# Kernel tuning notes

Measured on AMD Instinct MI355X. Metric: run time of the kernel, lower is better.

## Reference

```python
import jax, jax.numpy as jnp
import numpy as np

N = 4096      # num nodes/docs (<= max_compare=5000, so no random subsampling)
IN = 768      # input feature dim
OUT = 512     # projector output dim
TEM = 0.5     # temperature
BN_EPS = 1e-5
NORM_EPS = 1e-12


def setup_inputs() -> dict:
    key = jax.random.key(0)
    ks = jax.random.split(key, 5)
    doc0 = jax.random.normal(ks[0], (N, IN), dtype=jnp.float32)
    doc1 = jax.random.normal(ks[1], (N, IN), dtype=jnp.float32)
    doc2 = jax.random.normal(ks[2], (N, IN), dtype=jnp.float32)
    # 6 freshly-initialized projectors (one per view per pair, as in the torch forward)
    W1s = jax.random.normal(ks[3], (6, IN, OUT), dtype=jnp.float32) * 0.05
    b1s = jnp.zeros((6, OUT), dtype=jnp.float32)
    gammas = jnp.ones((6, OUT), dtype=jnp.float32)
    betas = jnp.zeros((6, OUT), dtype=jnp.float32)
    W2s = jax.random.normal(ks[4], (6, OUT, OUT), dtype=jnp.float32) * 0.05
    b2s = jnp.zeros((6, OUT), dtype=jnp.float32)
    return {"doc0": doc0, "doc1": doc1, "doc2": doc2,
            "W1s": W1s, "b1s": b1s, "gammas": gammas, "betas": betas,
            "W2s": W2s, "b2s": b2s}


def _projector(x, W1, b1, g, b, W2, b2):
    # Linear -> BatchNorm1d (training-mode batch stats) -> ReLU -> Linear
    h = x @ W1 + b1
    mu = h.mean(axis=0)
    var = h.var(axis=0)  # biased, matching torch BN normalization
    h = (h - mu) * jax.lax.rsqrt(var + BN_EPS) * g + b
    h = jax.nn.relu(h)
    return h @ W2 + b2


def _l2norm(x):
    n = jnp.sqrt(jnp.sum(x * x, axis=1, keepdims=True))
    return x / jnp.maximum(n, NORM_EPS)


def _pair_loss(a, b):
    # a, b: [N, OUT], already L2-normalized.
    # Full-matrix form of the chunked batch_loss (mathematically identical).
    refl = jnp.exp((a @ a.T) / TEM)      # [N, N]
    between = jnp.exp((a @ b.T) / TEM)   # [N, N]
    pos = jnp.diagonal(between)
    denom = refl.sum(axis=1) + between.sum(axis=1) - jnp.diagonal(refl)
    return -jnp.log(pos / denom)


def reference(doc0, doc1, doc2, W1s, b1s, gammas, betas, W2s, b2s):
    docs = [doc0, doc1, doc2]
    pairs = [(0, 1), (0, 2), (1, 2)]
    total = jnp.float32(0.0)
    k = 0
    for (i, j) in pairs:
        o1 = _l2norm(_projector(docs[i], W1s[k], b1s[k], gammas[k], betas[k], W2s[k], b2s[k]))
        k += 1
        o2 = _l2norm(_projector(docs[j], W1s[k], b1s[k], gammas[k], betas[k], W2s[k], b2s[k]))
        k += 1
        l = 0.5 * (_pair_loss(o1, o2) + _pair_loss(o2, o1))
        total = total + l.mean()
    return total / 3.0
```

## Files before the change

### kernel.cpp

```cpp
#include <hip/hip_runtime.h>
#include <hip/hip_bf16.h>
#include <hip/hip_fp8.h>

#define N_ROWS 4096
#define IN_DIM 768
#define OUT_DIM 512


using bf16x8 = __attribute__((ext_vector_type(8))) short;
using f32x4  = __attribute__((ext_vector_type(4))) float;
using i64    = long;
using i64x2  = __attribute__((ext_vector_type(2))) long;

__device__ __constant__ int c_docmap[6] = {0, 1, 0, 2, 1, 2};

__device__ inline unsigned short f2bf(float f) {
    __hip_bfloat16 h = __float2bfloat16(f);
    return reinterpret_cast<unsigned short&>(h);
}
__device__ inline float bf2f(unsigned short u) {
    return __uint_as_float((unsigned int)u << 16);
}
__device__ inline unsigned char f2fp8(float f) {
    __hip_fp8_e4m3 t(f);
    return t.__x;
}
__device__ inline uint4 pack8bf(const float* v) {
    uint4 o;
    unsigned short* p = (unsigned short*)&o;
#pragma unroll
    for (int j = 0; j < 8; ++j) p[j] = f2bf(v[j]);
    return o;
}

__global__ __launch_bounds__(256) void prep(
    const float* __restrict__ d0, const float* __restrict__ d1,
    const float* __restrict__ d2, const float* __restrict__ W1s,
    const float* __restrict__ W2s, unsigned short* __restrict__ Xb,
    unsigned short* __restrict__ W1t, unsigned short* __restrict__ W2t,
    char* __restrict__ zbase) {
    int wunit = blockIdx.x * 4 + (threadIdx.x >> 6);
    int lane = threadIdx.x & 63;
    int lane15 = lane & 15, quad = lane >> 4;
    if (wunit < 18432) {
        int d = wunit / 6144, u = wunit % 6144;
        int gt = u / 24, kf = u % 24;
        const float* src = (d == 0) ? d0 : ((d == 1) ? d1 : d2);
        const float* s = src + (size_t)(gt * 16 + lane15) * IN_DIM + kf * 32 + quad * 8;
        float4 a = *(const float4*)s, b = *(const float4*)(s + 4);
        float v[8] = {a.x, a.y, a.z, a.w, b.x, b.y, b.z, b.w};
        *(uint4*)(Xb + (size_t)d * N_ROWS * IN_DIM + (size_t)u * 512 + lane * 8) = pack8bf(v);
    } else if (wunit < 23040) {
        int v0 = wunit - 18432;
        int z = v0 / 768, u = v0 % 768;
        int gt = u / 24, kf = u % 24;
        int n = gt * 16 + lane15;
        int k0 = kf * 32 + quad * 8;
        const float* W = W1s + (size_t)z * IN_DIM * OUT_DIM;
        float v[8];
#pragma unroll
        for (int j = 0; j < 8; ++j) v[j] = W[(size_t)(k0 + j) * OUT_DIM + n];
        *(uint4*)(W1t + (size_t)z * OUT_DIM * IN_DIM + (size_t)u * 512 + lane * 8) = pack8bf(v);
    } else if (wunit < 26112) {
        int v0 = wunit - 23040;
        int z = v0 / 512, u = v0 % 512;
        int gt = u / 16, kf = u % 16;
        int n = gt * 16 + lane15;
        int k0 = kf * 32 + quad * 8;
        const float* W = W2s + (size_t)z * OUT_DIM * OUT_DIM;
        float v[8];
#pragma unroll
        for (int j = 0; j < 8; ++j) v[j] = W[(size_t)(k0 + j) * OUT_DIM + n];
        *(uint4*)(W2t + (size_t)z * OUT_DIM * OUT_DIM + (size_t)u * 512 + lane * 8) = pack8bf(v);
    } else {
        size_t b = (size_t)(wunit - 26112) * 1024 + (size_t)lane * 16;
        if (b < (size_t)(24576 + 98304))
            *(float4*)(zbase + b) = (float4){0.f, 0.f, 0.f, 0.f};
    }
}

__global__ __launch_bounds__(256) void gemm1_bn(
    const unsigned short* __restrict__ Xb, const unsigned short* __restrict__ W1t,
    const float* __restrict__ biasAll, unsigned short* __restrict__ H,
    float* __restrict__ stats) {
    const int NKF = IN_DIM / 32;
    int px = blockIdx.x;
    int logical = (px & 7) * 96 + (px >> 3);
    int T = logical >> 1, sub = logical & 1;
    int z = T >> 6, rem = T & 63;
    int m0 = (rem >> 2) * 256, n0 = (rem & 3) * 128;
    const unsigned short* A = Xb + (size_t)c_docmap[z] * N_ROWS * IN_DIM;
    const unsigned short* B = W1t + (size_t)z * OUT_DIM * IN_DIM;
    const float* bz = biasAll + (size_t)z * OUT_DIM;
    unsigned short* C = H + (size_t)z * N_ROWS * OUT_DIM;

    int tid = threadIdx.x;
    int wave = (tid >> 6) + sub * 4, lane = tid & 63;
    int lane15 = lane & 15, quad = lane >> 4;
    int wrow = (wave >> 1) * 64, wcol = (wave & 1) * 64;

    const unsigned short* Ca = A + (size_t)((m0 + wrow) >> 4) * NKF * 512 + (size_t)lane * 8;
    const unsigned short* Cb = B + (size_t)((n0 + wcol) >> 4) * NKF * 512 + (size_t)lane * 8;

    f32x4 acc[4][4];
#pragma unroll
    for (int mt = 0; mt < 4; ++mt)
#pragma unroll
        for (int nt = 0; nt < 4; ++nt)
            acc[mt][nt] = (f32x4){0.f, 0.f, 0.f, 0.f};

    bf16x8 aC[4], bC[4], aN[4], bN[4];
#pragma unroll
    for (int t = 0; t < 4; ++t) {
        aC[t] = *(const bf16x8*)(Ca + (size_t)t * NKF * 512);
        bC[t] = *(const bf16x8*)(Cb + (size_t)t * NKF * 512);
    }
#pragma unroll
    for (int kf = 0; kf < NKF; ++kf) {
        if (kf < NKF - 1) {
#pragma unroll
            for (int t = 0; t < 4; ++t) {
                aN[t] = *(const bf16x8*)(Ca + (size_t)t * NKF * 512 + (kf + 1) * 512);
                bN[t] = *(const bf16x8*)(Cb + (size_t)t * NKF * 512 + (kf + 1) * 512);
            }
        }
        __builtin_amdgcn_s_setprio(1);
#pragma unroll
        for (int mt = 0; mt < 4; ++mt)
#pragma unroll
            for (int nt = 0; nt < 4; ++nt)
                acc[mt][nt] = __builtin_amdgcn_mfma_f32_16x16x32_bf16(aC[mt], bC[nt], acc[mt][nt], 0, 0, 0);
        __builtin_amdgcn_s_setprio(0);
#pragma unroll
        for (int t = 0; t < 4; ++t) { aC[t] = aN[t]; bC[t] = bN[t]; }
    }

    float s1[4] = {0.f, 0.f, 0.f, 0.f}, s2[4] = {0.f, 0.f, 0.f, 0.f};
#pragma unroll
    for (int nt = 0; nt < 4; ++nt) {
        int col = n0 + wcol + nt * 16 + lane15;
        float bv = bz[col];
#pragma unroll
        for (int mt = 0; mt < 4; ++mt)
#pragma unroll
            for (int r = 0; r < 4; ++r) {
                int row = m0 + wrow + mt * 16 + quad * 4 + r;
                float v = acc[mt][nt][r] + bv;
                C[(size_t)row * OUT_DIM + col] = f2bf(v);
                s1[nt] += v; s2[nt] += v * v;
            }
    }
#pragma unroll
    for (int nt = 0; nt < 4; ++nt) {
        float a = s1[nt], b = s2[nt];
        a += __shfl_xor(a, 16); a += __shfl_xor(a, 32);
        b += __shfl_xor(b, 16); b += __shfl_xor(b, 32);
        if (quad == 0) {
            int col = n0 + wcol + nt * 16 + lane15;
            atomicAdd(&stats[((size_t)z * OUT_DIM + col) * 2 + 0], a);
            atomicAdd(&stats[((size_t)z * OUT_DIM + col) * 2 + 1], b);
        }
    }
}

__global__ __launch_bounds__(256) void bn_apply(
    const unsigned short* __restrict__ H, unsigned short* __restrict__ Hb,
    const float* __restrict__ stats, const float* __restrict__ gammas,
    const float* __restrict__ betas) {
    int wunit = blockIdx.x * 4 + (threadIdx.x >> 6);
    if (wunit >= 24576) return;
    int lane = threadIdx.x & 63;
    int lane15 = lane & 15, quad = lane >> 4;
    int z = wunit / 4096, u = wunit % 4096;
    int gt = u / 16, kf = u % 16;
    int row = gt * 16 + lane15;
    int k = kf * 32 + quad * 8;
    uint4 hu = *(const uint4*)(H + ((size_t)z * N_ROWS + row) * OUT_DIM + k);
    unsigned int w[4] = {hu.x, hu.y, hu.z, hu.w};
    float v[8];
#pragma unroll
    for (int j = 0; j < 8; ++j) {
        unsigned short us = (j & 1) ? (unsigned short)(w[j >> 1] >> 16)
                                    : (unsigned short)(w[j >> 1] & 0xffff);
        size_t sc = (size_t)z * OUT_DIM + k + j;
        float mu = stats[sc * 2 + 0] * (1.f / N_ROWS);
        float var = stats[sc * 2 + 1] * (1.f / N_ROWS) - mu * mu;
        float s = gammas[sc] * rsqrtf(var + 1e-5f);
        v[j] = fmaxf(fmaf(bf2f(us), s, betas[sc] - mu * s), 0.f);
    }
    *(uint4*)(Hb + (size_t)z * N_ROWS * OUT_DIM + (size_t)u * 512 + lane * 8) = pack8bf(v);
}

__global__ __launch_bounds__(512) void gemm2_fused(
    const unsigned short* __restrict__ Hb, const unsigned short* __restrict__ W2t,
    const float* __restrict__ biasAll, unsigned char* __restrict__ Abuf) {
    const int NKF = OUT_DIM / 32;
    int px = blockIdx.x;
    int L = (px & 7) * 48 + (px >> 3);
    int z = L >> 6;
    int m0 = (L & 63) * 64;
    const unsigned short* A = Hb + (size_t)z * N_ROWS * OUT_DIM;
    const unsigned short* B = W2t + (size_t)z * OUT_DIM * OUT_DIM;
    const float* bz = biasAll + (size_t)z * OUT_DIM;
    unsigned char* Az = Abuf + (size_t)z * N_ROWS * OUT_DIM;

    int tid = threadIdx.x;
    int wave = tid >> 6, lane = tid & 63;
    int lane15 = lane & 15, quad = lane >> 4;
    int wcol = wave * 64;

    const unsigned short* Ca = A + (size_t)(m0 >> 4) * NKF * 512 + (size_t)lane * 8;
    const unsigned short* Cb = B + (size_t)(wave * 4) * NKF * 512 + (size_t)lane * 8;

    f32x4 acc[4][4];
#pragma unroll
    for (int mt = 0; mt < 4; ++mt)
#pragma unroll
        for (int nt = 0; nt < 4; ++nt)
            acc[mt][nt] = (f32x4){0.f, 0.f, 0.f, 0.f};

    bf16x8 aC[4], bC[4], aN[4], bN[4];
#pragma unroll
    for (int t = 0; t < 4; ++t) {
        aC[t] = *(const bf16x8*)(Ca + (size_t)t * NKF * 512);
        bC[t] = *(const bf16x8*)(Cb + (size_t)t * NKF * 512);
    }
#pragma unroll
    for (int kf = 0; kf < NKF; ++kf) {
        if (kf < NKF - 1) {
#pragma unroll
            for (int t = 0; t < 4; ++t) {
                aN[t] = *(const bf16x8*)(Ca + (size_t)t * NKF * 512 + (kf + 1) * 512);
                bN[t] = *(const bf16x8*)(Cb + (size_t)t * NKF * 512 + (kf + 1) * 512);
            }
        }
#pragma unroll
        for (int mt = 0; mt < 4; ++mt)
#pragma unroll
            for (int nt = 0; nt < 4; ++nt)
                acc[mt][nt] = __builtin_amdgcn_mfma_f32_16x16x32_bf16(aC[mt], bC[nt], acc[mt][nt], 0, 0, 0);
#pragma unroll
        for (int t = 0; t < 4; ++t) { aC[t] = aN[t]; bC[t] = bN[t]; }
    }

    __shared__ float part[8][64];
    __shared__ float scf[64];
    __shared__ __attribute__((aligned(16))) unsigned char T[64 * 520];

    float rs[16];
#pragma unroll
    for (int j = 0; j < 16; ++j) rs[j] = 0.f;
#pragma unroll
    for (int nt = 0; nt < 4; ++nt) {
        float bv = bz[wcol + nt * 16 + lane15];
#pragma unroll
        for (int mt = 0; mt < 4; ++mt)
#pragma unroll
            for (int r = 0; r < 4; ++r) {
                float v = acc[mt][nt][r] + bv;
                acc[mt][nt][r] = v;
                rs[mt * 4 + r] += v * v;
            }
    }
#pragma unroll
    for (int j = 0; j < 16; ++j) {
        float v = rs[j];
        v += __shfl_xor(v, 1); v += __shfl_xor(v, 2);
        v += __shfl_xor(v, 4); v += __shfl_xor(v, 8);
        rs[j] = v;
    }
    if (lane15 == 0) {
#pragma unroll
        for (int j = 0; j < 16; ++j)
            part[wave][(j >> 2) * 16 + quad * 4 + (j & 3)] = rs[j];
    }
    __syncthreads();
    if (tid < 64) {
        float ss = 0.f;
#pragma unroll
        for (int w = 0; w < 8; ++w) ss += part[w][tid];
        scf[tid] = 1.f / fmaxf(sqrtf(ss), 1e-12f);
    }
    __syncthreads();
#pragma unroll
    for (int mt = 0; mt < 4; ++mt)
#pragma unroll
        for (int r = 0; r < 4; ++r) {
            int row = mt * 16 + quad * 4 + r;
            float s = scf[row];
#pragma unroll
            for (int nt = 0; nt < 4; ++nt)
                T[row * 520 + wcol + nt * 16 + lane15] = f2fp8(acc[mt][nt][r] * s);
        }
    __syncthreads();
#pragma unroll
    for (int gt = 0; gt < 4; ++gt) {
        int row = gt * 16 + lane15;
        i64 lo = *(const i64*)(T + row * 520 + (2 * wave) * 32 + quad * 8);
        i64 hi = *(const i64*)(T + row * 520 + (2 * wave + 1) * 32 + quad * 8);
        i64x2 st; st[0] = lo; st[1] = hi;
        int gtg = (m0 >> 4) + gt;
        *(i64x2*)(Az + ((size_t)(gtg * 8 + wave) * 64 + lane) * 16) = st;
    }
}

__global__ __launch_bounds__(256, 3) void gram_kernel(const unsigned char* __restrict__ Abase,
                                                      float* __restrict__ rowsum,
                                                      float* __restrict__ crossdot) {
    int px = blockIdx.x;
    int logical = (px & 7) * 792 + (px >> 3);
    int tile = logical >> 1, sub = logical & 1;
    int p = tile / 1056;
    int t0 = tile - p * 1056;
    const unsigned char* Cm = Abase + (size_t)p * 2 * N_ROWS * OUT_DIM;

    int I = 0;
    while (t0 >= 64 - 2 * I) { t0 -= 64 - 2 * I; ++I; }
    int J = 2 * I + t0;
    int m0 = I * 256, n0 = J * 128;

    int tid = threadIdx.x;
    int wave = (tid >> 6) + sub * 4, lane = tid & 63;
    int lane15 = lane & 15, quad = lane >> 4;
    int wrow = (wave >> 1) * 64, wcol = (wave & 1) * 64;

    const unsigned char* Ca = Cm + (size_t)((m0 + wrow) >> 4) * 8192 + (size_t)lane * 16;
    const unsigned char* Cb = Cm + (size_t)((n0 + wcol) >> 4) * 8192 + (size_t)lane * 16;

    f32x4 acc[4][4];
#pragma unroll
    for (int mt = 0; mt < 4; ++mt)
#pragma unroll
        for (int nt = 0; nt < 4; ++nt)
            acc[mt][nt] = (f32x4){0.f, 0.f, 0.f, 0.f};

#pragma unroll 1
    for (int kh = 0; kh < 8; ++kh) {
        i64x2 a[4], b[4];
#pragma unroll
        for (int t = 0; t < 4; ++t) {
            a[t] = *(const i64x2*)(Ca + (size_t)t * 8192 + (size_t)kh * 1024);
            b[t] = *(const i64x2*)(Cb + (size_t)t * 8192 + (size_t)kh * 1024);
        }
#pragma unroll
        for (int half = 0; half < 2; ++half)
#pragma unroll
            for (int mt = 0; mt < 4; ++mt)
#pragma unroll
                for (int nt = 0; nt < 4; ++nt)
                    acc[mt][nt] = __builtin_amdgcn_mfma_f32_16x16x32_fp8_fp8(
                        a[mt][half], b[nt][half], acc[mt][nt], 0, 0, 0);
    }

    float* cdp = crossdot + (size_t)p * 2 * N_ROWS;
    float* rp  = rowsum  + (size_t)p * 2 * N_ROWS;

    float rs[16];
    float cs[4] = {0.f, 0.f, 0.f, 0.f};
#pragma unroll
    for (int j = 0; j < 16; ++j) rs[j] = 0.f;

    if (J >= 2 * I + 2) {
#pragma unroll
        for (int mt = 0; mt < 4; ++mt)
#pragma unroll
            for (int nt = 0; nt < 4; ++nt)
#pragma unroll
                for (int r = 0; r < 4; ++r) {
                    float e = __expf(2.f * acc[mt][nt][r]);
                    rs[mt * 4 + r] += e;
                    cs[nt] += e;
                }
        if (J >= 32 && ((J - 32) >> 1) == I) {
#pragma unroll
            for (int mt = 0; mt < 4; ++mt)
#pragma unroll
                for (int nt = 0; nt < 4; ++nt) {
                    int gcol = n0 + wcol + nt * 16 + lane15;
#pragma unroll
                    for (int r = 0; r < 4; ++r) {
                        int grow = m0 + wrow + mt * 16 + quad * 4 + r;
                        if (gcol == grow + N_ROWS) {
                            float s = acc[mt][nt][r];
                            cdp[grow] = s;
                            cdp[gcol] = s;
                        }
                    }
                }
        }
    } else {
#pragma unroll
        for (int mt = 0; mt < 4; ++mt)
#pragma unroll
            for (int nt = 0; nt < 4; ++nt) {
                int gcol = n0 + wcol + nt * 16 + lane15;
#pragma unroll
                for (int r = 0; r < 4; ++r) {
                    int grow = m0 + wrow + mt * 16 + quad * 4 + r;
                    if (grow < gcol) {
                        float e = __expf(2.f * acc[mt][nt][r]);
                        rs[mt * 4 + r] += e;
                        cs[nt] += e;
                    }
                }
            }
    }

#pragma unroll
    for (int j = 0; j < 16; ++j) {
        float v = rs[j];
        v += __shfl_xor(v, 1); v += __shfl_xor(v, 2);
        v += __shfl_xor(v, 4); v += __shfl_xor(v, 8);
        rs[j] = v;
    }
    if (lane15 == 0) {
#pragma unroll
        for (int j = 0; j < 16; ++j) {
            int grow = m0 + wrow + (j >> 2) * 16 + quad * 4 + (j & 3);
            atomicAdd(&rp[grow], rs[j]);
        }
    }
#pragma unroll
    for (int n = 0; n < 4; ++n) {
        float v = cs[n];
        v += __shfl_xor(v, 16); v += __shfl_xor(v, 32);
        cs[n] = v;
    }
    if (quad == 0) {
#pragma unroll
        for (int n = 0; n < 4; ++n) {
            int gcol = n0 + wcol + n * 16 + lane15;
            atomicAdd(&rp[gcol], cs[n]);
        }
    }
}

__global__ void loss_kernel(const float* __restrict__ rowsum,
                            const float* __restrict__ crossdot, float* __restrict__ out) {
    int i = blockIdx.x * 256 + threadIdx.x;
    float v = logf(rowsum[i]) - 2.f * crossdot[i];
#pragma unroll
    for (int m = 1; m < 64; m <<= 1) v += __shfl_xor(v, m);
    __shared__ float red[4];
    if ((threadIdx.x & 63) == 0) red[threadIdx.x >> 6] = v;
    __syncthreads();
    if (threadIdx.x == 0)
        atomicAdd(out, (red[0] + red[1] + red[2] + red[3]) * (1.f / 24576.f));
}

extern "C" void kernel_launch(void* const* d_in, const int* in_sizes, int n_in,
                              void* d_out, int out_size, void* d_ws, size_t ws_size,
                              hipStream_t stream) {
    const float* doc0   = (const float*)d_in[0];
    const float* doc1   = (const float*)d_in[1];
    const float* doc2   = (const float*)d_in[2];
    const float* W1s    = (const float*)d_in[3];
    const float* b1s    = (const float*)d_in[4];
    const float* gammas = (const float*)d_in[5];
    const float* betas  = (const float*)d_in[6];
    const float* W2s    = (const float*)d_in[7];
    const float* b2s    = (const float*)d_in[8];
    float* out = (float*)d_out;

    char* base = (char*)d_ws;
    size_t off = 0;
    auto alloc = [&](size_t bytes) -> char* {
        char* r = base + off;
        off += (bytes + 255) & ~(size_t)255;
        return r;
    };

    unsigned short* Xb   = (unsigned short*)alloc((size_t)3 * N_ROWS * IN_DIM * 2);
    unsigned short* W1t  = (unsigned short*)alloc((size_t)6 * OUT_DIM * IN_DIM * 2);
    unsigned short* W2t  = (unsigned short*)alloc((size_t)6 * OUT_DIM * OUT_DIM * 2);
    unsigned short* H    = (unsigned short*)alloc((size_t)6 * N_ROWS * OUT_DIM * 2);
    unsigned short* Hb   = (unsigned short*)alloc((size_t)6 * N_ROWS * OUT_DIM * 2);
    unsigned char*  Abuf = (unsigned char*)Xb;
    char* zbase = alloc(24576 + 98304);
    float* stats  = (float*)zbase;
    float* rowsum = (float*)(zbase + 24576);
    float* cdot   = (float*)alloc((size_t)3 * 2 * N_ROWS * 4);

    if (ws_size < off) return;

    hipMemsetAsync(out, 0, sizeof(float), stream);

    prep<<<6558, 256, 0, stream>>>(doc0, doc1, doc2, W1s, W2s, Xb, W1t, W2t, zbase);

    gemm1_bn<<<768, 256, 0, stream>>>(Xb, W1t, b1s, H, stats);

    bn_apply<<<6144, 256, 0, stream>>>(H, Hb, stats, gammas, betas);

    gemm2_fused<<<384, 512, 0, stream>>>(Hb, W2t, b2s, Abuf);

    gram_kernel<<<6336, 256, 0, stream>>>(Abuf, rowsum, cdot);

    loss_kernel<<<96, 256, 0, stream>>>(rowsum, cdot, out);
}
```

Baseline: 283.8 us.

## Stage gram tiles in double-buffered LDS via direct global-to-LDS loads

The gram kernel now runs one 256x128 tile per 512-thread block instead of splitting it across two 256-thread blocks. The block cooperatively streams the A and B fp8 panels into a double-buffered LDS area with global_load_lds, prefetching the next k-slice while MFMAs run. This lets the waves that share a tile reuse the same data and stop issuing redundant global loads. It also raises wave priority around the MFMA section. In exchange it adds 48KB of LDS per block and a barrier every k-step, which may limit occupancy.

```diff
diff --git a/kernel.cpp b/kernel.cpp
--- a/kernel.cpp
+++ b/kernel.cpp
@@ -304,14 +304,13 @@
     }
 }
 
-__global__ __launch_bounds__(256, 3) void gram_kernel(const unsigned char* __restrict__ Abase,
+__global__ __launch_bounds__(512, 4) void gram_kernel(const unsigned char* __restrict__ Abase,
                                                       float* __restrict__ rowsum,
                                                       float* __restrict__ crossdot) {
     int px = blockIdx.x;
-    int logical = (px & 7) * 792 + (px >> 3);
-    int tile = logical >> 1, sub = logical & 1;
-    int p = tile / 1056;
-    int t0 = tile - p * 1056;
+    int logical = (px & 7) * 396 + (px >> 3);
+    int p = logical / 1056;
+    int t0 = logical - p * 1056;
     const unsigned char* Cm = Abase + (size_t)p * 2 * N_ROWS * OUT_DIM;
 
     int I = 0;
@@ -320,12 +319,32 @@
     int m0 = I * 256, n0 = J * 128;
 
     int tid = threadIdx.x;
-    int wave = (tid >> 6) + sub * 4, lane = tid & 63;
+    int wave = tid >> 6, lane = tid & 63;
     int lane15 = lane & 15, quad = lane >> 4;
     int wrow = (wave >> 1) * 64, wcol = (wave & 1) * 64;
 
-    const unsigned char* Ca = Cm + (size_t)((m0 + wrow) >> 4) * 8192 + (size_t)lane * 16;
-    const unsigned char* Cb = Cm + (size_t)((n0 + wcol) >> 4) * 8192 + (size_t)lane * 16;
+    __shared__ __attribute__((aligned(16))) unsigned char lds[2][24 * 1024];
+
+    const unsigned char* gA = Cm + (size_t)(m0 >> 4) * 8192;
+    const unsigned char* gB = Cm + (size_t)(n0 >> 4) * 8192;
+    const unsigned char* gsrc[3];
+    int cdst[3];
+#pragma unroll
+    for (int j = 0; j < 3; ++j) {
+        int c = wave * 3 + j;
+        gsrc[j] = ((c < 16) ? (gA + (size_t)c * 8192) : (gB + (size_t)(c - 16) * 8192))
+                  + (size_t)lane * 16;
+        cdst[j] = c * 1024;
+    }
+
+    typedef __attribute__((address_space(1))) const unsigned int gu32;
+    typedef __attribute__((address_space(3))) unsigned int su32;
+
+#pragma unroll
+    for (int j = 0; j < 3; ++j)
+        __builtin_amdgcn_global_load_lds((gu32*)(const void*)gsrc[j],
+                                         (su32*)(void*)(&lds[0][cdst[j]]), 16, 0, 0);
+    __syncthreads();
 
     f32x4 acc[4][4];
 #pragma unroll
@@ -334,14 +353,26 @@
         for (int nt = 0; nt < 4; ++nt)
             acc[mt][nt] = (f32x4){0.f, 0.f, 0.f, 0.f};
 
+    int aoff = (wrow >> 4) * 1024 + lane * 16;
+    int boff = (16 + (wcol >> 4)) * 1024 + lane * 16;
+
 #pragma unroll 1
     for (int kh = 0; kh < 8; ++kh) {
+        int cur = kh & 1;
+        if (kh < 7) {
+#pragma unroll
+            for (int j = 0; j < 3; ++j)
+                __builtin_amdgcn_global_load_lds(
+                    (gu32*)(const void*)(gsrc[j] + (size_t)(kh + 1) * 1024),
+                    (su32*)(void*)(&lds[cur ^ 1][cdst[j]]), 16, 0, 0);
+        }
         i64x2 a[4], b[4];
 #pragma unroll
         for (int t = 0; t < 4; ++t) {
-            a[t] = *(const i64x2*)(Ca + (size_t)t * 8192 + (size_t)kh * 1024);
-            b[t] = *(const i64x2*)(Cb + (size_t)t * 8192 + (size_t)kh * 1024);
-        }
+            a[t] = *(const i64x2*)(&lds[cur][aoff + t * 1024]);
+            b[t] = *(const i64x2*)(&lds[cur][boff + t * 1024]);
+        }
+        __builtin_amdgcn_s_setprio(1);
 #pragma unroll
         for (int half = 0; half < 2; ++half)
 #pragma unroll
@@ -350,6 +381,8 @@
                 for (int nt = 0; nt < 4; ++nt)
                     acc[mt][nt] = __builtin_amdgcn_mfma_f32_16x16x32_fp8_fp8(
                         a[mt][half], b[nt][half], acc[mt][nt], 0, 0, 0);
+        __builtin_amdgcn_s_setprio(0);
+        __syncthreads();
     }
 
     float* cdp = crossdot + (size_t)p * 2 * N_ROWS;
@@ -493,7 +526,7 @@
 
     gemm2_fused<<<384, 512, 0, stream>>>(Hb, W2t, b2s, Abuf);
 
-    gram_kernel<<<6336, 256, 0, stream>>>(Abuf, rowsum, cdot);
+    gram_kernel<<<3168, 512, 0, stream>>>(Abuf, rowsum, cdot);
 
     loss_kernel<<<96, 256, 0, stream>>>(rowsum, cdot, out);
 }
```

Result: faster. 276.8 us (-2.5%).
